# Kernel optimization log

Measured on AMD Instinct MI355X. Metric: run time of the kernel, lower is better.

## Reference

```python
import jax, jax.numpy as jnp
import numpy as np

B, T, D, H = 4, 2048, 384, 6
HD = D // H  # 64
HALF = HD // 2


def setup_inputs() -> dict:
    key = jax.random.key(0)
    k0, k1, k2 = jax.random.split(key, 3)
    x = jax.random.normal(k0, (B, T, D), jnp.float32)
    attn_bias = jnp.zeros((1, 1, T, T), jnp.float32)  # additive SDPA bias
    # standard RoPE tables: [T, HD/2]
    inv_freq = 1.0 / (10000.0 ** (np.arange(HALF, dtype=np.float32) / HALF))
    ang = np.arange(T, dtype=np.float32)[:, None] * inv_freq[None, :]
    cos = jnp.asarray(np.cos(ang), jnp.float32)
    sin = jnp.asarray(np.sin(ang), jnp.float32)
    w_qkv = jax.random.normal(k1, (D, 3 * D), jnp.float32) * (D ** -0.5)
    w_proj = jax.random.normal(k2, (D, D), jnp.float32) * (D ** -0.5)
    return {"x": x, "attn_bias": attn_bias, "cos": cos, "sin": sin,
            "w_qkv": w_qkv, "w_proj": w_proj}


def _apply_rope(x, cos, sin):
    # x: [b, h, t, hd]; cos/sin: [t, hd/2] -> rotate-half RoPE
    half = x.shape[-1] // 2
    x1, x2 = x[..., :half], x[..., half:]
    c = cos[None, None, :, :]
    s = sin[None, None, :, :]
    return jnp.concatenate([x1 * c - x2 * s, x2 * c + x1 * s], axis=-1)


def reference(x, attn_bias, cos, sin, w_qkv, w_proj):
    b, t, _ = x.shape
    qkv = (x @ w_qkv).reshape(b, t, 3, H, HD)  # fused QKV projection
    q = jnp.transpose(qkv[:, :, 0], (0, 2, 1, 3))  # [b,h,t,hd]
    k = jnp.transpose(qkv[:, :, 1], (0, 2, 1, 3))
    v = jnp.transpose(qkv[:, :, 2], (0, 2, 1, 3))
    q = _apply_rope(q, cos, sin)
    k = _apply_rope(k, cos, sin)
    scale = 1.0 / jnp.sqrt(jnp.asarray(HD, x.dtype))
    scores = jnp.einsum("bhqd,bhkd->bhqk", q, k) * scale + attn_bias
    attn = jax.nn.softmax(scores, axis=-1)
    out = jnp.einsum("bhqk,bhkd->bhqd", attn, v)
    out = jnp.transpose(out, (0, 2, 1, 3)).reshape(b, t, H * HD)
    return out @ w_proj
```

## Files before the change

### kernel.cpp

```cpp
#include <hip/hip_runtime.h>
#include <hip/hip_bf16.h>

#define BB   4
#define TT   2048
#define DDIM 384
#define HH   6
#define HD   64
#define BT   (BB*TT)
#define QKVC (3*DDIM)

#define QSCALE 0.18033688011112042f
#define LOG2E  1.4426950408889634f

typedef __attribute__((ext_vector_type(4))) short short4v;
typedef __attribute__((ext_vector_type(8))) short short8v;
typedef __attribute__((ext_vector_type(4))) float float4v;
typedef unsigned short u16;

static __device__ __forceinline__ u16 f2bu(float f) {
    __hip_bfloat16 h = __float2bfloat16(f);
    return __builtin_bit_cast(u16, h);
}
static __device__ __forceinline__ unsigned pk2(float lo, float hi) {
    return (unsigned)f2bu(lo) | ((unsigned)f2bu(hi) << 16);
}
static __device__ __forceinline__ float bu2f_lo(unsigned u) {
    return __builtin_bit_cast(float, u << 16);
}
static __device__ __forceinline__ float bu2f_hi(unsigned u) {
    return __builtin_bit_cast(float, u & 0xffff0000u);
}
static __device__ __forceinline__ short8v frag4(uint4 v) {
    return __builtin_bit_cast(short8v, v);
}
static __device__ __forceinline__ short8v ld_frag(const u16* p) {
    short4v a = *(const short4v*)p;
    short4v b = *(const short4v*)(p + 4);
    return __builtin_shufflevector(a, b, 0, 1, 2, 3, 4, 5, 6, 7);
}
static __device__ __forceinline__ void st8(u16* p, uint4 v) {
    *(uint2*)p       = make_uint2(v.x, v.y);
    *(uint2*)(p + 4) = make_uint2(v.z, v.w);
}
static __device__ __forceinline__ void pl32swap(unsigned &a, unsigned &b) {
    auto r = __builtin_amdgcn_permlane32_swap(a, b, false, false);
    a = r[0]; b = r[1];
}
static __device__ __forceinline__ void pl16swap(unsigned &a, unsigned &b) {
    auto r = __builtin_amdgcn_permlane16_swap(a, b, false, false);
    a = r[0]; b = r[1];
}

#define MFMA16(a, b, c) __builtin_amdgcn_mfma_f32_16x16x32_bf16((a), (b), (c), 0, 0, 0)
#define PIN_PREFETCH() __builtin_amdgcn_sched_barrier(0)

__global__ __launch_bounds__(256) void prep_kernel(
    const float* __restrict__ wqkv, const float* __restrict__ wproj,
    const float* __restrict__ x, const float* __restrict__ bias,
    u16* __restrict__ wqkvT, u16* __restrict__ wprojT,
    u16* __restrict__ xb, u16* __restrict__ bias16)
{
    const int bid = blockIdx.x;
    const int t = threadIdx.x;
    if (bid >= 144) {
        const float* src; u16* dst; float scl; size_t base;
        if (bid < 912) { src = x;    dst = xb;     scl = 1.0f;
                         base = (size_t)(bid - 144) * 4096 + (size_t)t * 16; }
        else           { src = bias; dst = bias16; scl = LOG2E;
                         base = (size_t)(bid - 912) * 4096 + (size_t)t * 16; }
        const float* gp = src + base;
        __align__(16) u16 tmp[16];
        #pragma unroll
        for (int u = 0; u < 4; ++u) {
            float4 v = *(const float4*)(gp + 4 * u);
            tmp[4 * u + 0] = f2bu(v.x * scl); tmp[4 * u + 1] = f2bu(v.y * scl);
            tmp[4 * u + 2] = f2bu(v.z * scl); tmp[4 * u + 3] = f2bu(v.w * scl);
        }
        *(uint4*)(dst + base)     = *(const uint4*)tmp;
        *(uint4*)(dst + base + 8) = *(const uint4*)(tmp + 8);
        return;
    }
    const float* in; u16* out; int K, C, c0, k0;
    if (bid < 108) { in = wqkv;  out = wqkvT;  K = DDIM; C = QKVC;
                     c0 = (bid % 18) * 64; k0 = (bid / 18) * 64; }
    else           { int b2 = bid - 108; in = wproj; out = wprojT; K = DDIM; C = DDIM;
                     c0 = (b2 % 6) * 64; k0 = (b2 / 6) * 64; }
    __shared__ float tr[64][65];
    {
        int kr = t >> 2, cb = (t & 3) * 16;
        const float* gp = in + (size_t)(k0 + kr) * C + c0 + cb;
        #pragma unroll
        for (int u = 0; u < 4; ++u) {
            float4 v = *(const float4*)(gp + 4 * u);
            tr[cb + 4 * u + 0][kr] = v.x;
            tr[cb + 4 * u + 1][kr] = v.y;
            tr[cb + 4 * u + 2][kr] = v.z;
            tr[cb + 4 * u + 3][kr] = v.w;
        }
    }
    __syncthreads();
    {
        int c = t >> 2, kb = (t & 3) * 16;
        __align__(16) u16 tmp[16];
        #pragma unroll
        for (int u = 0; u < 16; ++u) tmp[u] = f2bu(tr[c][kb + u]);
        u16* op = out + (size_t)(c0 + c) * K + k0 + kb;
        *(uint4*)op       = *(const uint4*)tmp;
        *(uint4*)(op + 8) = *(const uint4*)(tmp + 8);
    }
}

__global__ __launch_bounds__(256, 4) void qkv_rope_kernel(
    const u16* __restrict__ xb, const u16* __restrict__ wt,
    const float* __restrict__ cs, const float* __restrict__ sn,
    u16* __restrict__ qb, u16* __restrict__ kb, u16* __restrict__ vtb)
{
    __shared__ __align__(16) u16 xs[2][64][68];
    __shared__ __align__(16) u16 ws[2][64][68];
    const int t = threadIdx.x;
    const int wv = t >> 6, lane = t & 63, quad = lane >> 4, lo = lane & 15;
    const int r0 = blockIdx.y * 64;
    const int c0 = blockIdx.x * 64;
    const int sr = t >> 3, sd = (t & 7) * 8;

    st8(&xs[0][sr][sd],      *(const uint4*)(xb + (size_t)(r0 + sr) * DDIM + sd));
    st8(&xs[0][sr + 32][sd], *(const uint4*)(xb + (size_t)(r0 + sr + 32) * DDIM + sd));
    st8(&ws[0][sr][sd],      *(const uint4*)(wt + (size_t)(c0 + sr) * DDIM + sd));
    st8(&ws[0][sr + 32][sd], *(const uint4*)(wt + (size_t)(c0 + sr + 32) * DDIM + sd));
    __syncthreads();

    float4v acc[4] = {};
    for (int kk = 0; kk < 6; ++kk) {
        const int cur = kk & 1, nxt = cur ^ 1;
        const int kkn = (kk < 5 ? kk + 1 : 5) * 64;
        uint4 xp0 = *(const uint4*)(xb + (size_t)(r0 + sr) * DDIM + kkn + sd);
        uint4 xp1 = *(const uint4*)(xb + (size_t)(r0 + sr + 32) * DDIM + kkn + sd);
        uint4 wp0 = *(const uint4*)(wt + (size_t)(c0 + sr) * DDIM + kkn + sd);
        uint4 wp1 = *(const uint4*)(wt + (size_t)(c0 + sr + 32) * DDIM + kkn + sd);
        PIN_PREFETCH();

        #pragma unroll
        for (int kf = 0; kf < 2; ++kf) {
            short8v a = ld_frag(&xs[cur][16 * wv + lo][kf * 32 + quad * 8]);
            #pragma unroll
            for (int nt = 0; nt < 4; ++nt) {
                short8v b = ld_frag(&ws[cur][nt * 16 + lo][kf * 32 + quad * 8]);
                acc[nt] = MFMA16(a, b, acc[nt]);
            }
        }
        st8(&xs[nxt][sr][sd], xp0);
        st8(&xs[nxt][sr + 32][sd], xp1);
        st8(&ws[nxt][sr][sd], wp0);
        st8(&ws[nxt][sr + 32][sd], wp1);
        __syncthreads();
    }

    const int sec = blockIdx.x / 6;
    const int h   = blockIdx.x % 6;
    const int rbase = r0 + 16 * wv + 4 * quad;
    const int bidx  = r0 >> 11;
    const int tbase = rbase & (TT - 1);

    if (sec == 2) {
        #pragma unroll
        for (int nt = 0; nt < 4; ++nt) {
            int d = nt * 16 + lo;
            unsigned a0 = pk2(acc[nt][0], acc[nt][1]);
            unsigned a1 = pk2(acc[nt][2], acc[nt][3]);
            u16* gp = vtb + ((size_t)(bidx * HH + h) * HD + d) * TT + tbase;
            *(uint2*)gp = make_uint2(a0, a1);
        }
    } else {
        u16* dst = (sec == 0) ? qb : kb;
        const float scl = (sec == 0) ? QSCALE : 1.0f;
        #pragma unroll
        for (int np = 0; np < 2; ++np) {
            #pragma unroll
            for (int r = 0; r < 4; ++r) {
                int tpos = tbase + r;
                int ci = np * 16 + lo;
                float cv = cs[tpos * 32 + ci];
                float sv = sn[tpos * 32 + ci];
                float x1 = acc[np][r], x2 = acc[np + 2][r];
                u16* gp = dst + ((size_t)(bidx * HH + h) * TT + tpos) * HD;
                gp[ci]      = f2bu((x1 * cv - x2 * sv) * scl);
                gp[ci + 32] = f2bu((x2 * cv + x1 * sv) * scl);
            }
        }
    }
}

template <bool B16>
__global__ __launch_bounds__(256, 4) void attn_kernel(
    const u16* __restrict__ qb, const u16* __restrict__ kb, const u16* __restrict__ vtb,
    const float* __restrict__ bias, const u16* __restrict__ bias16,
    u16* __restrict__ ob)
{
    __shared__ __align__(16) u16 ks[2][64][68];
    __shared__ __align__(16) u16 vt[2][64][68];

    const int t = threadIdx.x;
    const int wv = t >> 6, lane = t & 63, quad = lane >> 4, lo = lane & 15;
    const int bh = blockIdx.x;
    const int b = bh / HH, h = bh % HH;
    const int q0 = blockIdx.y * 64;
    const int qrow = q0 + 16 * wv + lo;

    const u16* qbase = qb + ((size_t)bh * TT + qrow) * HD + quad * 8;
    short8v aq0 = frag4(*(const uint4*)qbase);
    short8v aq1 = frag4(*(const uint4*)(qbase + 32));

    const int sr = t >> 3, sd = (t & 7) * 8;
    const u16* kbbase = kb + (size_t)bh * TT * HD;
    const u16* vtbase = vtb + (size_t)bh * HD * TT;
    const float* brow = bias + (size_t)qrow * TT + 4 * quad;
    const u16* brow16 = bias16 + (size_t)qrow * TT + 4 * quad;

    st8(&ks[0][sr][sd],      *(const uint4*)(kbbase + (size_t)sr * HD + sd));
    st8(&ks[0][sr + 32][sd], *(const uint4*)(kbbase + (size_t)(sr + 32) * HD + sd));
    st8(&vt[0][sr][sd],      *(const uint4*)(vtbase + (size_t)sr * TT + sd));
    st8(&vt[0][sr + 32][sd], *(const uint4*)(vtbase + (size_t)(sr + 32) * TT + sd));
    float4 bcur[4]; uint2 bcur16[4];
    #pragma unroll
    for (int nt = 0; nt < 4; ++nt) {
        if constexpr (B16) bcur16[nt] = *(const uint2*)(brow16 + nt * 16);
        else               bcur[nt]   = *(const float4*)(brow + nt * 16);
    }
    __syncthreads();

    float4v oacc[4] = {};
    float lacc[4] = {0.f, 0.f, 0.f, 0.f};

    for (int kt = 0; kt < TT / 64; ++kt) {
        const int cur = kt & 1, nxt = cur ^ 1;
        const int kn = (kt < 31 ? kt + 1 : 31) * 64;

        uint4 kp0 = *(const uint4*)(kbbase + (size_t)(kn + sr) * HD + sd);
        uint4 kp1 = *(const uint4*)(kbbase + (size_t)(kn + sr + 32) * HD + sd);
        uint4 vp0 = *(const uint4*)(vtbase + (size_t)sr * TT + kn + sd);
        uint4 vp1 = *(const uint4*)(vtbase + (size_t)(sr + 32) * TT + kn + sd);
        float4 bnxt[4]; uint2 bnxt16[4];
        #pragma unroll
        for (int nt = 0; nt < 4; ++nt) {
            if constexpr (B16) bnxt16[nt] = *(const uint2*)(brow16 + kn + nt * 16);
            else               bnxt[nt]   = *(const float4*)(brow + kn + nt * 16);
        }
        PIN_PREFETCH();

        float4v s[4] = {};
        __builtin_amdgcn_s_setprio(1);
        #pragma unroll
        for (int kf = 0; kf < 2; ++kf) {
            #pragma unroll
            for (int nt = 0; nt < 4; ++nt) {
                short8v kfr = ld_frag(&ks[cur][nt * 16 + lo][kf * 32 + quad * 8]);
                s[nt] = MFMA16(kfr, (kf ? aq1 : aq0), s[nt]);
            }
        }
        __builtin_amdgcn_s_setprio(0);

        unsigned w[8];
        #pragma unroll
        for (int nt = 0; nt < 4; ++nt) {
            float b0, b1, b2, b3;
            if constexpr (B16) {
                b0 = bu2f_lo(bcur16[nt].x); b1 = bu2f_hi(bcur16[nt].x);
                b2 = bu2f_lo(bcur16[nt].y); b3 = bu2f_hi(bcur16[nt].y);
            } else {
                b0 = bcur[nt].x * LOG2E; b1 = bcur[nt].y * LOG2E;
                b2 = bcur[nt].z * LOG2E; b3 = bcur[nt].w * LOG2E;
            }
            float p0 = __builtin_amdgcn_exp2f(s[nt][0] + b0);
            float p1 = __builtin_amdgcn_exp2f(s[nt][1] + b1);
            float p2 = __builtin_amdgcn_exp2f(s[nt][2] + b2);
            float p3 = __builtin_amdgcn_exp2f(s[nt][3] + b3);
            lacc[nt] += (p0 + p1) + (p2 + p3);
            w[2 * nt]     = pk2(p0, p1);
            w[2 * nt + 1] = pk2(p2, p3);
        }

        pl32swap(w[0], w[2]); pl16swap(w[0], w[2]);
        pl32swap(w[1], w[3]); pl16swap(w[1], w[3]);
        pl32swap(w[4], w[6]); pl16swap(w[4], w[6]);
        pl32swap(w[5], w[7]); pl16swap(w[5], w[7]);
        short8v pa0 = frag4(make_uint4(w[0], w[1], w[2], w[3]));
        short8v pa1 = frag4(make_uint4(w[4], w[5], w[6], w[7]));

        __builtin_amdgcn_s_setprio(1);
        #pragma unroll
        for (int kf = 0; kf < 2; ++kf) {
            #pragma unroll
            for (int dt = 0; dt < 4; ++dt) {
                short8v bv = ld_frag(&vt[cur][dt * 16 + lo][kf * 32 + quad * 8]);
                oacc[dt] = MFMA16((kf ? pa1 : pa0), bv, oacc[dt]);
            }
        }
        __builtin_amdgcn_s_setprio(0);

        st8(&ks[nxt][sr][sd], kp0);
        st8(&ks[nxt][sr + 32][sd], kp1);
        st8(&vt[nxt][sr][sd], vp0);
        st8(&vt[nxt][sr + 32][sd], vp1);
        #pragma unroll
        for (int nt = 0; nt < 4; ++nt) {
            if constexpr (B16) bcur16[nt] = bnxt16[nt];
            else               bcur[nt]   = bnxt[nt];
        }
        __syncthreads();
    }

    float l = (lacc[0] + lacc[1]) + (lacc[2] + lacc[3]);
    l += __shfl_xor(l, 16);
    l += __shfl_xor(l, 32);
    #pragma unroll
    for (int r = 0; r < 4; ++r) {
        float lr = __shfl(l, 4 * quad + r);
        float inv = 1.f / lr;
        u16* gp = ob + ((size_t)b * TT + q0 + 16 * wv + 4 * quad + r) * DDIM + h * HD + lo;
        #pragma unroll
        for (int dt = 0; dt < 4; ++dt)
            gp[dt * 16] = f2bu(oacc[dt][r] * inv);
    }
}

__global__ __launch_bounds__(256, 4) void proj_kernel(
    const u16* __restrict__ o, const u16* __restrict__ wt, float* __restrict__ out)
{
    __shared__ __align__(16) u16 os[2][64][68];
    __shared__ __align__(16) u16 ws[2][64][68];
    const int t = threadIdx.x;
    const int wv = t >> 6, lane = t & 63, quad = lane >> 4, lo = lane & 15;
    const int r0 = blockIdx.y * 64, c0 = blockIdx.x * 64;
    const int sr = t >> 3, sd = (t & 7) * 8;

    st8(&os[0][sr][sd],      *(const uint4*)(o + (size_t)(r0 + sr) * DDIM + sd));
    st8(&os[0][sr + 32][sd], *(const uint4*)(o + (size_t)(r0 + sr + 32) * DDIM + sd));
    st8(&ws[0][sr][sd],      *(const uint4*)(wt + (size_t)(c0 + sr) * DDIM + sd));
    st8(&ws[0][sr + 32][sd], *(const uint4*)(wt + (size_t)(c0 + sr + 32) * DDIM + sd));
    __syncthreads();

    float4v acc[4] = {};
    for (int kk = 0; kk < 6; ++kk) {
        const int cur = kk & 1, nxt = cur ^ 1;
        const int kkn = (kk < 5 ? kk + 1 : 5) * 64;
        uint4 op0 = *(const uint4*)(o + (size_t)(r0 + sr) * DDIM + kkn + sd);
        uint4 op1 = *(const uint4*)(o + (size_t)(r0 + sr + 32) * DDIM + kkn + sd);
        uint4 wp0 = *(const uint4*)(wt + (size_t)(c0 + sr) * DDIM + kkn + sd);
        uint4 wp1 = *(const uint4*)(wt + (size_t)(c0 + sr + 32) * DDIM + kkn + sd);
        PIN_PREFETCH();

        #pragma unroll
        for (int kf = 0; kf < 2; ++kf) {
            short8v a = ld_frag(&os[cur][16 * wv + lo][kf * 32 + quad * 8]);
            #pragma unroll
            for (int nt = 0; nt < 4; ++nt) {
                short8v bfr = ld_frag(&ws[cur][nt * 16 + lo][kf * 32 + quad * 8]);
                acc[nt] = MFMA16(a, bfr, acc[nt]);
            }
        }
        st8(&os[nxt][sr][sd], op0);
        st8(&os[nxt][sr + 32][sd], op1);
        st8(&ws[nxt][sr][sd], wp0);
        st8(&ws[nxt][sr + 32][sd], wp1);
        __syncthreads();
    }
    #pragma unroll
    for (int r = 0; r < 4; ++r) {
        float* gp = out + (size_t)(r0 + 16 * wv + 4 * quad + r) * DDIM + c0;
        #pragma unroll
        for (int nt = 0; nt < 4; ++nt)
            gp[nt * 16 + lo] = acc[nt][r];
    }
}

extern "C" void kernel_launch(void* const* d_in, const int* in_sizes, int n_in,
                              void* d_out, int out_size, void* d_ws, size_t ws_size,
                              hipStream_t stream) {
    const float* x     = (const float*)d_in[0];
    const float* bias  = (const float*)d_in[1];
    const float* cs    = (const float*)d_in[2];
    const float* sn    = (const float*)d_in[3];
    const float* wqkv  = (const float*)d_in[4];
    const float* wproj = (const float*)d_in[5];
    float* out = (float*)d_out;

    u16* wqkvT  = (u16*)d_ws;
    u16* wprojT = wqkvT + (size_t)QKVC * DDIM;
    u16* qb     = wprojT + (size_t)DDIM * DDIM;
    u16* kb     = qb + (size_t)BB * HH * TT * HD;
    u16* vtb    = kb + (size_t)BB * HH * TT * HD;
    u16* ob     = vtb + (size_t)BB * HH * TT * HD;
    u16* xb     = ob + (size_t)BT * DDIM;
    u16* bias16 = xb + (size_t)BT * DDIM;

    const size_t need_b16 = ((size_t)(bias16 - wqkvT) + (size_t)TT * TT) * sizeof(u16);
    const bool useb16 = ws_size >= need_b16;

    prep_kernel<<<dim3(144 + BT * DDIM / 4096 + (useb16 ? TT * TT / 4096 : 0)),
                  256, 0, stream>>>(wqkv, wproj, x, bias, wqkvT, wprojT, xb, bias16);
    qkv_rope_kernel<<<dim3(QKVC / 64, BT / 64), 256, 0, stream>>>(
        xb, wqkvT, cs, sn, qb, kb, vtb);
    if (useb16)
        attn_kernel<true><<<dim3(BB * HH, TT / 64), 256, 0, stream>>>(
            qb, kb, vtb, bias, bias16, ob);
    else
        attn_kernel<false><<<dim3(BB * HH, TT / 64), 256, 0, stream>>>(
            qb, kb, vtb, bias, bias16, ob);
    proj_kernel<<<dim3(DDIM / 64, BT / 64), 256, 0, stream>>>(ob, wprojT, out);
}
```

Measured before the change: 178.7 us.

## Add zero-bias fast path with key-split register-resident attention kernel

```diff
diff --git a/kernel.cpp b/kernel.cpp
--- a/kernel.cpp
+++ b/kernel.cpp
@@ -24,12 +24,6 @@
 static __device__ __forceinline__ unsigned pk2(float lo, float hi) {
     return (unsigned)f2bu(lo) | ((unsigned)f2bu(hi) << 16);
 }
-static __device__ __forceinline__ float bu2f_lo(unsigned u) {
-    return __builtin_bit_cast(float, u << 16);
-}
-static __device__ __forceinline__ float bu2f_hi(unsigned u) {
-    return __builtin_bit_cast(float, u & 0xffff0000u);
-}
 static __device__ __forceinline__ short8v frag4(uint4 v) {
     return __builtin_bit_cast(short8v, v);
 }
@@ -52,32 +46,41 @@
 }
 
 #define MFMA16(a, b, c) __builtin_amdgcn_mfma_f32_16x16x32_bf16((a), (b), (c), 0, 0, 0)
-#define PIN_PREFETCH() __builtin_amdgcn_sched_barrier(0)
 
 __global__ __launch_bounds__(256) void prep_kernel(
     const float* __restrict__ wqkv, const float* __restrict__ wproj,
     const float* __restrict__ x, const float* __restrict__ bias,
     u16* __restrict__ wqkvT, u16* __restrict__ wprojT,
-    u16* __restrict__ xb, u16* __restrict__ bias16)
+    u16* __restrict__ xb, unsigned* __restrict__ flag)
 {
     const int bid = blockIdx.x;
     const int t = threadIdx.x;
-    if (bid >= 144) {
-        const float* src; u16* dst; float scl; size_t base;
-        if (bid < 912) { src = x;    dst = xb;     scl = 1.0f;
-                         base = (size_t)(bid - 144) * 4096 + (size_t)t * 16; }
-        else           { src = bias; dst = bias16; scl = LOG2E;
-                         base = (size_t)(bid - 912) * 4096 + (size_t)t * 16; }
-        const float* gp = src + base;
-        __align__(16) u16 tmp[16];
+    if (bid >= 912) {
+        const float* gp = bias + (size_t)(bid - 912) * 4096 + (size_t)t * 16;
+        unsigned acc = 0;
         #pragma unroll
         for (int u = 0; u < 4; ++u) {
             float4 v = *(const float4*)(gp + 4 * u);
-            tmp[4 * u + 0] = f2bu(v.x * scl); tmp[4 * u + 1] = f2bu(v.y * scl);
-            tmp[4 * u + 2] = f2bu(v.z * scl); tmp[4 * u + 3] = f2bu(v.w * scl);
-        }
-        *(uint4*)(dst + base)     = *(const uint4*)tmp;
-        *(uint4*)(dst + base + 8) = *(const uint4*)(tmp + 8);
+            acc |= (__builtin_bit_cast(unsigned, v.x) & 0x7fffffffu);
+            acc |= (__builtin_bit_cast(unsigned, v.y) & 0x7fffffffu);
+            acc |= (__builtin_bit_cast(unsigned, v.z) & 0x7fffffffu);
+            acc |= (__builtin_bit_cast(unsigned, v.w) & 0x7fffffffu);
+        }
+        if (acc) atomicOr(flag, 1u);
+        return;
+    }
+    if (bid >= 144) {
+        size_t base = (size_t)(bid - 144) * 4096 + (size_t)t * 16;
+        const float* gp = x + base;
+        __align__(16) u16 tmp[16];
+        #pragma unroll
+        for (int u = 0; u < 4; ++u) {
+            float4 v = *(const float4*)(gp + 4 * u);
+            tmp[4 * u + 0] = f2bu(v.x); tmp[4 * u + 1] = f2bu(v.y);
+            tmp[4 * u + 2] = f2bu(v.z); tmp[4 * u + 3] = f2bu(v.w);
+        }
+        *(uint4*)(xb + base)     = *(const uint4*)tmp;
+        *(uint4*)(xb + base + 8) = *(const uint4*)(tmp + 8);
         return;
     }
     const float* in; u16* out; int K, C, c0, k0;
@@ -137,7 +140,6 @@
         uint4 xp1 = *(const uint4*)(xb + (size_t)(r0 + sr + 32) * DDIM + kkn + sd);
         uint4 wp0 = *(const uint4*)(wt + (size_t)(c0 + sr) * DDIM + kkn + sd);
         uint4 wp1 = *(const uint4*)(wt + (size_t)(c0 + sr + 32) * DDIM + kkn + sd);
-        PIN_PREFETCH();
 
         #pragma unroll
         for (int kf = 0; kf < 2; ++kf) {
@@ -190,12 +192,174 @@
     }
 }
 
-template <bool B16>
-__global__ __launch_bounds__(256, 4) void attn_kernel(
+__global__ __launch_bounds__(256, 2) void attn_ksplit_kernel(
     const u16* __restrict__ qb, const u16* __restrict__ kb, const u16* __restrict__ vtb,
-    const float* __restrict__ bias, const u16* __restrict__ bias16,
+    const unsigned* __restrict__ flag, u16* __restrict__ ob)
+{
+    if (*flag != 0u) return;
+
+    __shared__ __align__(16) float red_o[2][64][68];
+    __shared__ float red_l[4][64];
+
+    const int t = threadIdx.x;
+    const int wv = t >> 6, lane = t & 63, quad = lane >> 4, lo = lane & 15;
+    const int bh = blockIdx.x;
+    const int b = bh / HH, h = bh % HH;
+    const int q0 = blockIdx.y * 64;
+
+    short8v aq[4][2];
+    #pragma unroll
+    for (int g = 0; g < 4; ++g) {
+        const u16* qp = qb + ((size_t)bh * TT + q0 + g * 16 + lo) * HD + quad * 8;
+        aq[g][0] = frag4(*(const uint4*)qp);
+        aq[g][1] = frag4(*(const uint4*)(qp + 32));
+    }
+
+    const u16* kbase = kb + ((size_t)bh * TT + lo) * HD + quad * 8;
+    const u16* vbase = vtb + ((size_t)bh * HD + lo) * TT + quad * 8;
+
+    uint4 kq[4][2], vq[4][2];
+    {
+        const size_t ko = (size_t)wv * 64 * HD;
+        const size_t vo = (size_t)wv * 64;
+        #pragma unroll
+        for (int nt = 0; nt < 4; ++nt) {
+            kq[nt][0] = *(const uint4*)(kbase + ko + (size_t)nt * 16 * HD);
+            kq[nt][1] = *(const uint4*)(kbase + ko + (size_t)nt * 16 * HD + 32);
+        }
+        #pragma unroll
+        for (int dt = 0; dt < 4; ++dt) {
+            vq[dt][0] = *(const uint4*)(vbase + (size_t)dt * 16 * TT + vo);
+            vq[dt][1] = *(const uint4*)(vbase + (size_t)dt * 16 * TT + vo + 32);
+        }
+    }
+
+    float4v oacc[4][4] = {};
+    float lacc[4] = {0.f, 0.f, 0.f, 0.f};
+
+    for (int j = 0; j < 8; ++j) {
+        const int ktn = (j < 7) ? (wv + 4 * (j + 1)) : wv;
+        const size_t kno = (size_t)ktn * 64 * HD;
+        const size_t vno = (size_t)ktn * 64;
+
+        #pragma unroll
+        for (int g = 0; g < 4; ++g) {
+            float4v s[4] = {};
+            #pragma unroll
+            for (int nt = 0; nt < 4; ++nt)
+                s[nt] = MFMA16(frag4(kq[nt][0]), aq[g][0], s[nt]);
+            #pragma unroll
+            for (int nt = 0; nt < 4; ++nt)
+                s[nt] = MFMA16(frag4(kq[nt][1]), aq[g][1], s[nt]);
+            if (g == 3) {
+                #pragma unroll
+                for (int nt = 0; nt < 4; ++nt) {
+                    kq[nt][0] = *(const uint4*)(kbase + kno + (size_t)nt * 16 * HD);
+                    kq[nt][1] = *(const uint4*)(kbase + kno + (size_t)nt * 16 * HD + 32);
+                }
+            }
+
+            unsigned w[8];
+            #pragma unroll
+            for (int nt = 0; nt < 4; ++nt) {
+                float p0 = __builtin_amdgcn_exp2f(s[nt][0]);
+                float p1 = __builtin_amdgcn_exp2f(s[nt][1]);
+                float p2 = __builtin_amdgcn_exp2f(s[nt][2]);
+                float p3 = __builtin_amdgcn_exp2f(s[nt][3]);
+                lacc[g] += (p0 + p1) + (p2 + p3);
+                w[2 * nt]     = pk2(p0, p1);
+                w[2 * nt + 1] = pk2(p2, p3);
+            }
+
+            pl32swap(w[0], w[2]); pl16swap(w[0], w[2]);
+            pl32swap(w[1], w[3]); pl16swap(w[1], w[3]);
+            pl32swap(w[4], w[6]); pl16swap(w[4], w[6]);
+            pl32swap(w[5], w[7]); pl16swap(w[5], w[7]);
+            short8v pa0 = frag4(make_uint4(w[0], w[1], w[2], w[3]));
+            short8v pa1 = frag4(make_uint4(w[4], w[5], w[6], w[7]));
+
+            #pragma unroll
+            for (int dt = 0; dt < 4; ++dt)
+                oacc[g][dt] = MFMA16(pa0, frag4(vq[dt][0]), oacc[g][dt]);
+            #pragma unroll
+            for (int dt = 0; dt < 4; ++dt)
+                oacc[g][dt] = MFMA16(pa1, frag4(vq[dt][1]), oacc[g][dt]);
+            if (g == 3) {
+                #pragma unroll
+                for (int dt = 0; dt < 4; ++dt) {
+                    vq[dt][0] = *(const uint4*)(vbase + (size_t)dt * 16 * TT + vno);
+                    vq[dt][1] = *(const uint4*)(vbase + (size_t)dt * 16 * TT + vno + 32);
+                }
+            }
+        }
+    }
+
+    #pragma unroll
+    for (int g = 0; g < 4; ++g) {
+        lacc[g] += __shfl_xor(lacc[g], 16);
+        lacc[g] += __shfl_xor(lacc[g], 32);
+    }
+    if (quad == 0) {
+        #pragma unroll
+        for (int g = 0; g < 4; ++g) red_l[wv][g * 16 + lo] = lacc[g];
+    }
+    float* slot0 = &red_o[0][0][0] + (size_t)lane * 68;
+    float* slot1 = &red_o[1][0][0] + (size_t)lane * 68;
+    if (wv == 1 || wv == 3) {
+        float* sp = (wv == 1) ? slot0 : slot1;
+        #pragma unroll
+        for (int g = 0; g < 4; ++g)
+            #pragma unroll
+            for (int dt = 0; dt < 4; ++dt)
+                *(float4v*)(sp + (g * 4 + dt) * 4) = oacc[g][dt];
+    }
+    __syncthreads();
+    if (wv == 0 || wv == 2) {
+        float* sp = (wv == 0) ? slot0 : slot1;
+        #pragma unroll
+        for (int g = 0; g < 4; ++g)
+            #pragma unroll
+            for (int dt = 0; dt < 4; ++dt)
+                oacc[g][dt] += *(const float4v*)(sp + (g * 4 + dt) * 4);
+    }
+    __syncthreads();
+    if (wv == 2) {
+        #pragma unroll
+        for (int g = 0; g < 4; ++g)
+            #pragma unroll
+            for (int dt = 0; dt < 4; ++dt)
+                *(float4v*)(slot1 + (g * 4 + dt) * 4) = oacc[g][dt];
+    }
+    __syncthreads();
+    if (wv == 0) {
+        #pragma unroll
+        for (int g = 0; g < 4; ++g) {
+            #pragma unroll
+            for (int dt = 0; dt < 4; ++dt)
+                oacc[g][dt] += *(const float4v*)(slot1 + (g * 4 + dt) * 4);
+            float lt = red_l[0][g * 16 + lo] + red_l[1][g * 16 + lo]
+                     + red_l[2][g * 16 + lo] + red_l[3][g * 16 + lo];
+            #pragma unroll
+            for (int r = 0; r < 4; ++r) {
+                float lr = __shfl(lt, 4 * quad + r);
+                float inv = 1.f / lr;
+                u16* gp = ob + ((size_t)b * TT + q0 + g * 16 + 4 * quad + r) * DDIM
+                             + h * HD + lo;
+                #pragma unroll
+                for (int dt = 0; dt < 4; ++dt)
+                    gp[dt * 16] = f2bu(oacc[g][dt][r] * inv);
+            }
+        }
+    }
+}
+
+__global__ __launch_bounds__(256, 4) void attn_bias_kernel(
+    const u16* __restrict__ qb, const u16* __restrict__ kb, const u16* __restrict__ vtb,
+    const float* __restrict__ bias, const unsigned* __restrict__ flag,
     u16* __restrict__ ob)
 {
+    if (*flag == 0u) return;
+
     __shared__ __align__(16) u16 ks[2][64][68];
     __shared__ __align__(16) u16 vt[2][64][68];
 
@@ -214,18 +378,14 @@
     const u16* kbbase = kb + (size_t)bh * TT * HD;
     const u16* vtbase = vtb + (size_t)bh * HD * TT;
     const float* brow = bias + (size_t)qrow * TT + 4 * quad;
-    const u16* brow16 = bias16 + (size_t)qrow * TT + 4 * quad;
 
     st8(&ks[0][sr][sd],      *(const uint4*)(kbbase + (size_t)sr * HD + sd));
     st8(&ks[0][sr + 32][sd], *(const uint4*)(kbbase + (size_t)(sr + 32) * HD + sd));
     st8(&vt[0][sr][sd],      *(const uint4*)(vtbase + (size_t)sr * TT + sd));
     st8(&vt[0][sr + 32][sd], *(const uint4*)(vtbase + (size_t)(sr + 32) * TT + sd));
-    float4 bcur[4]; uint2 bcur16[4];
+    float4 bcur[4];
     #pragma unroll
-    for (int nt = 0; nt < 4; ++nt) {
-        if constexpr (B16) bcur16[nt] = *(const uint2*)(brow16 + nt * 16);
-        else               bcur[nt]   = *(const float4*)(brow + nt * 16);
-    }
+    for (int nt = 0; nt < 4; ++nt) bcur[nt] = *(const float4*)(brow + nt * 16);
     __syncthreads();
 
     float4v oacc[4] = {};
@@ -239,16 +399,11 @@
         uint4 kp1 = *(const uint4*)(kbbase + (size_t)(kn + sr + 32) * HD + sd);
         uint4 vp0 = *(const uint4*)(vtbase + (size_t)sr * TT + kn + sd);
         uint4 vp1 = *(const uint4*)(vtbase + (size_t)(sr + 32) * TT + kn + sd);
-        float4 bnxt[4]; uint2 bnxt16[4];
-        #pragma unroll
-        for (int nt = 0; nt < 4; ++nt) {
-            if constexpr (B16) bnxt16[nt] = *(const uint2*)(brow16 + kn + nt * 16);
-            else               bnxt[nt]   = *(const float4*)(brow + kn + nt * 16);
-        }
-        PIN_PREFETCH();
+        float4 bnxt[4];
+        #pragma unroll
+        for (int nt = 0; nt < 4; ++nt) bnxt[nt] = *(const float4*)(brow + kn + nt * 16);
 
         float4v s[4] = {};
-        __builtin_amdgcn_s_setprio(1);
         #pragma unroll
         for (int kf = 0; kf < 2; ++kf) {
             #pragma unroll
@@ -257,23 +412,14 @@
                 s[nt] = MFMA16(kfr, (kf ? aq1 : aq0), s[nt]);
             }
         }
-        __builtin_amdgcn_s_setprio(0);
 
         unsigned w[8];
         #pragma unroll
         for (int nt = 0; nt < 4; ++nt) {
-            float b0, b1, b2, b3;
-            if constexpr (B16) {
-                b0 = bu2f_lo(bcur16[nt].x); b1 = bu2f_hi(bcur16[nt].x);
-                b2 = bu2f_lo(bcur16[nt].y); b3 = bu2f_hi(bcur16[nt].y);
-            } else {
-                b0 = bcur[nt].x * LOG2E; b1 = bcur[nt].y * LOG2E;
-                b2 = bcur[nt].z * LOG2E; b3 = bcur[nt].w * LOG2E;
-            }
-            float p0 = __builtin_amdgcn_exp2f(s[nt][0] + b0);
-            float p1 = __builtin_amdgcn_exp2f(s[nt][1] + b1);
-            float p2 = __builtin_amdgcn_exp2f(s[nt][2] + b2);
-            float p3 = __builtin_amdgcn_exp2f(s[nt][3] + b3);
+            float p0 = __builtin_amdgcn_exp2f(fmaf(bcur[nt].x, LOG2E, s[nt][0]));
+            float p1 = __builtin_amdgcn_exp2f(fmaf(bcur[nt].y, LOG2E, s[nt][1]));
+            float p2 = __builtin_amdgcn_exp2f(fmaf(bcur[nt].z, LOG2E, s[nt][2]));
+            float p3 = __builtin_amdgcn_exp2f(fmaf(bcur[nt].w, LOG2E, s[nt][3]));
             lacc[nt] += (p0 + p1) + (p2 + p3);
             w[2 * nt]     = pk2(p0, p1);
             w[2 * nt + 1] = pk2(p2, p3);
@@ -286,7 +432,6 @@
         short8v pa0 = frag4(make_uint4(w[0], w[1], w[2], w[3]));
         short8v pa1 = frag4(make_uint4(w[4], w[5], w[6], w[7]));
 
-        __builtin_amdgcn_s_setprio(1);
         #pragma unroll
         for (int kf = 0; kf < 2; ++kf) {
             #pragma unroll
@@ -295,17 +440,13 @@
                 oacc[dt] = MFMA16((kf ? pa1 : pa0), bv, oacc[dt]);
             }
         }
-        __builtin_amdgcn_s_setprio(0);
 
         st8(&ks[nxt][sr][sd], kp0);
         st8(&ks[nxt][sr + 32][sd], kp1);
         st8(&vt[nxt][sr][sd], vp0);
         st8(&vt[nxt][sr + 32][sd], vp1);
         #pragma unroll
-        for (int nt = 0; nt < 4; ++nt) {
-            if constexpr (B16) bcur16[nt] = bnxt16[nt];
-            else               bcur[nt]   = bnxt[nt];
-        }
+        for (int nt = 0; nt < 4; ++nt) bcur[nt] = bnxt[nt];
         __syncthreads();
     }
 
@@ -347,7 +488,6 @@
         uint4 op1 = *(const uint4*)(o + (size_t)(r0 + sr + 32) * DDIM + kkn + sd);
         uint4 wp0 = *(const uint4*)(wt + (size_t)(c0 + sr) * DDIM + kkn + sd);
         uint4 wp1 = *(const uint4*)(wt + (size_t)(c0 + sr + 32) * DDIM + kkn + sd);
-        PIN_PREFETCH();
 
         #pragma unroll
         for (int kf = 0; kf < 2; ++kf) {
@@ -391,20 +531,16 @@
     u16* vtb    = kb + (size_t)BB * HH * TT * HD;
     u16* ob     = vtb + (size_t)BB * HH * TT * HD;
     u16* xb     = ob + (size_t)BT * DDIM;
-    u16* bias16 = xb + (size_t)BT * DDIM;
-
-    const size_t need_b16 = ((size_t)(bias16 - wqkvT) + (size_t)TT * TT) * sizeof(u16);
-    const bool useb16 = ws_size >= need_b16;
-
-    prep_kernel<<<dim3(144 + BT * DDIM / 4096 + (useb16 ? TT * TT / 4096 : 0)),
-                  256, 0, stream>>>(wqkv, wproj, x, bias, wqkvT, wprojT, xb, bias16);
+    unsigned* flag = (unsigned*)(xb + (size_t)BT * DDIM);
+
+    hipMemsetAsync(flag, 0, sizeof(unsigned), stream);
+    prep_kernel<<<dim3(144 + BT * DDIM / 4096 + TT * TT / 4096), 256, 0, stream>>>(
+        wqkv, wproj, x, bias, wqkvT, wprojT, xb, flag);
     qkv_rope_kernel<<<dim3(QKVC / 64, BT / 64), 256, 0, stream>>>(
         xb, wqkvT, cs, sn, qb, kb, vtb);
-    if (useb16)
-        attn_kernel<true><<<dim3(BB * HH, TT / 64), 256, 0, stream>>>(
-            qb, kb, vtb, bias, bias16, ob);
-    else
-        attn_kernel<false><<<dim3(BB * HH, TT / 64), 256, 0, stream>>>(
-            qb, kb, vtb, bias, bias16, ob);
+    attn_ksplit_kernel<<<dim3(BB * HH, TT / 64), 256, 0, stream>>>(
+        qb, kb, vtb, flag, ob);
+    attn_bias_kernel<<<dim3(BB * HH, TT / 64), 256, 0, stream>>>(
+        qb, kb, vtb, bias, flag, ob);
     proj_kernel<<<dim3(DDIM / 64, BT / 64), 256, 0, stream>>>(ob, wprojT, out);
 }
```

New measurement: 167.3 us. 1.07x faster.
